# Performance work log

Measured on AMD Instinct MI355X. Metric: run time of the kernel, lower is better.

The kernel has to match this reference:

```python
import jax, jax.numpy as jnp
from jax import lax
import numpy as np

B, T, F, H, L = 256, 512, 16, 256, 2


def _lstm_layer(x, w_ih, w_hh, b_ih, b_hh):
    # x: [B, T, in]; w_ih: [4H, in]; w_hh: [4H, H]; biases: [4H]
    # PyTorch gate order: i, f, g, o
    x_proj = jnp.einsum('bti,gi->btg', x, w_ih) + b_ih + b_hh  # [B, T, 4H]
    h0 = jnp.zeros((x.shape[0], w_hh.shape[1]), x.dtype)
    c0 = h0

    def step(carry, xp):
        h, c = carry
        gates = xp + h @ w_hh.T  # [B, 4H]
        i, f, g, o = jnp.split(gates, 4, axis=-1)
        c = jax.nn.sigmoid(f) * c + jax.nn.sigmoid(i) * jnp.tanh(g)
        h = jax.nn.sigmoid(o) * jnp.tanh(c)
        return (h, c), h

    _, hs = lax.scan(step, (h0, c0), jnp.swapaxes(x_proj, 0, 1))  # [T, B, H]
    return jnp.swapaxes(hs, 0, 1)  # [B, T, H]


def setup_inputs() -> dict:
    key = jax.random.key(0)
    ks = jax.random.split(key, 16)
    x = jax.random.normal(ks[0], (B, T, F), dtype=jnp.float32)
    lengths = jax.random.randint(ks[1], (B,), 1, T + 1)  # in [1, T]
    s = 1.0 / np.sqrt(H)
    u = lambda k, shape: jax.random.uniform(k, shape, jnp.float32, -s, s)
    inp = {'x': x, 'lengths': lengths}
    in_dims = [F, H]
    for l in range(L):
        inp[f'w_ih{l}'] = u(ks[2 + 4 * l], (4 * H, in_dims[l]))
        inp[f'w_hh{l}'] = u(ks[3 + 4 * l], (4 * H, H))
        inp[f'b_ih{l}'] = u(ks[4 + 4 * l], (4 * H,))
        inp[f'b_hh{l}'] = u(ks[5 + 4 * l], (4 * H,))
    inp['fc_w'] = u(ks[10], (1, H))
    inp['fc_b'] = u(ks[11], (1,))
    return inp


def reference(x, lengths, w_ih0, w_hh0, b_ih0, b_hh0,
              w_ih1, w_hh1, b_ih1, b_hh1, fc_w, fc_b):
    # Packed LSTM: outputs at t >= length never influence last_outputs
    # (recurrence only flows forward in time), so running the dense
    # full-length LSTM and gathering at lengths-1 is mathematically identical.
    h = _lstm_layer(x, w_ih0, w_hh0, b_ih0, b_hh0)
    h = _lstm_layer(h, w_ih1, w_hh1, b_ih1, b_hh1)
    last = h[jnp.arange(h.shape[0]), lengths - 1]  # [B, H]
    return jax.nn.relu(last) @ fc_w.T + fc_b  # [B, 1]
```

## Files before the change

kernel.cpp:

```cpp
#include <hip/hip_runtime.h>
#include <hip/hip_fp16.h>


#define Tc 32
#define NCHUNK 16

#define OFF_IH0   0
#define OFF_B0    16384
#define OFF_B1    17408
#define OFF_C0S   18432
#define OFF_C1S   84480
#define OFF_H1S   150528
#define OFF_HLAST 216576
#define FP_END    282624
#define H_HH0  0
#define H_HH1  262144
#define H_IH1  524288
#define H_H0C  786432
#define H0SLOT 2113536
#define H_XP1  5013504
#define XPSLOT 8454144

#define SMEM_BYTES 66560

typedef _Float16 v2h __attribute__((ext_vector_type(2)));

__device__ __forceinline__ unsigned packh2(float a, float b) {
  __half2 h = __floats2half2_rn(a, b);
  return *(unsigned*)&h;
}
__device__ __forceinline__ float4 dot4(const float4 w, const v2h h, float4 acc) {
  const v2h* wg = (const v2h*)&w;
  acc.x = __builtin_amdgcn_fdot2(wg[0], h, acc.x, false);
  acc.y = __builtin_amdgcn_fdot2(wg[1], h, acc.y, false);
  acc.z = __builtin_amdgcn_fdot2(wg[2], h, acc.z, false);
  acc.w = __builtin_amdgcn_fdot2(wg[3], h, acc.w, false);
  return acc;
}
__device__ __forceinline__ float sigf(float x) {
  return __fdividef(1.f, 1.f + __expf(-x));
}
__device__ __forceinline__ float tanhf_fast(float x) {
  float ax = fabsf(x);
  float e = __expf(-2.f * ax);
  float t = __fdividef(1.f - e, 1.f + e);
  return copysignf(t, x);
}
__device__ __forceinline__ float4 f4fma(float4 a, float4 w, float s) {
  a.x = fmaf(w.x, s, a.x);
  a.y = fmaf(w.y, s, a.y);
  a.z = fmaf(w.z, s, a.z);
  a.w = fmaf(w.w, s, a.w);
  return a;
}
__device__ __forceinline__ float h2f(unsigned short s) {
  __half h = __builtin_bit_cast(__half, s);
  return __half2float(h);
}
__device__ __forceinline__ float4 cvt4(ushort4 v) {
  float4 r;
  r.x = h2f(v.x); r.y = h2f(v.y); r.z = h2f(v.z); r.w = h2f(v.w);
  return r;
}

__global__ __launch_bounds__(256) void prep_kernel(
    const float* __restrict__ w_ih0, const float* __restrict__ w_hh0,
    const float* __restrict__ b_ih0, const float* __restrict__ b_hh0,
    const float* __restrict__ w_ih1, const float* __restrict__ w_hh1,
    const float* __restrict__ b_ih1, const float* __restrict__ b_hh1,
    float* __restrict__ ws) {
  const int idx = blockIdx.x * blockDim.x + threadIdx.x;
  const int g = idx & 3, u = (idx >> 2) & 255, p = idx >> 10;
  const int j = g * 256 + u;
  unsigned* h16u = (unsigned*)(ws + FP_END);
  h16u[H_HH0 / 2 + idx] = packh2(w_hh0[j * 256 + 2 * p], w_hh0[j * 256 + 2 * p + 1]);
  h16u[H_HH1 / 2 + idx] = packh2(w_hh1[j * 256 + 2 * p], w_hh1[j * 256 + 2 * p + 1]);
  h16u[H_IH1 / 2 + idx] = packh2(w_ih1[j * 256 + 2 * p], w_ih1[j * 256 + 2 * p + 1]);
  if (idx < 16384) ws[OFF_IH0 + idx] = w_ih0[j * 16 + (idx >> 10)];
  if (idx < 1024) {
    ws[OFF_B0 + idx] = b_ih0[j] + b_hh0[j];
    ws[OFF_B1 + idx] = b_ih1[j] + b_hh1[j];
  }
}

__global__ __launch_bounds__(512) void fused_kernel(
    float* __restrict__ ws, const float* __restrict__ x,
    const int* __restrict__ lengths, int step) {
  extern __shared__ __align__(16) char smem_raw[];
  const int bid = blockIdx.x;
  const int tid = threadIdx.x;
  __half* h16 = (__half*)(ws + FP_END);
  unsigned short* h0cS = (unsigned short*)(h16 + H_H0C);
  unsigned short* xpS = (unsigned short*)(h16 + H_XP1);

  if (bid < 86) {
    if (step >= NCHUNK) return;
    const int kc = step;
    const int kh = tid >> 8, u = tid & 255;
    const int bg = bid * 3;
    unsigned short* hb = (unsigned short*)smem_raw;
    float* xsp = (float*)(smem_raw + 4096);
    float* scratch = (float*)(smem_raw + 4608);

    int len[3];
    #pragma unroll
    for (int b = 0; b < 3; ++b) len[b] = (bg + b < 256) ? lengths[bg + b] : 1;
    const int tmaxb = max(len[0], max(len[1], len[2]));
    if (kc * Tc >= tmaxb) return;
    const int tend = min(Tc, tmaxb - kc * Tc);
    const int slot = kc & 1, slotP = slot ^ 1;

    const float4* wq = (const float4*)(h16 + H_HH0) + (size_t)kh * 64 * 256 + u;
    const float4* wih = (const float4*)(ws + OFF_IH0) + kh * 8 * 256 + u;
    const float4 bias = ((const float4*)(ws + OFF_B0))[u];

    float c[3] = {0.f, 0.f, 0.f};
    if (kh == 0) {
      #pragma unroll
      for (int b = 0; b < 3; ++b) {
        unsigned short hv = 0;
        if (kc > 0) {
          hv = h0cS[(size_t)slotP * H0SLOT + ((size_t)(bg + b) * 32 + 31) * 256 + u];
          c[b] = ws[OFF_C0S + (bg + b) * 256 + u];
        }
        hb[0 * 768 + b * 256 + u] = hv;
      }
    }
    if (tid < 48) {
      int b = tid >> 4, i = tid & 15;
      int bb = min(bg + b, 255);
      xsp[0 * 48 + b * 16 + i] = x[(size_t)bb * 8192 + (kc * Tc) * 16 + i];
    }
    __syncthreads();

    for (int tc = 0; tc < tend; ++tc) {
      const int cur = tc & 1, nxt = cur ^ 1;
      float4 A0, A1, A2;
      if (kh == 0) { A0 = bias; A1 = bias; A2 = bias; }
      else { A0 = make_float4(0, 0, 0, 0); A1 = A0; A2 = A0; }

      #pragma unroll
      for (int ii = 0; ii < 8; ++ii) {
        float4 w = wih[ii * 256];
        A0 = f4fma(A0, w, xsp[cur * 48 + 0 * 16 + kh * 8 + ii]);
        A1 = f4fma(A1, w, xsp[cur * 48 + 1 * 16 + kh * 8 + ii]);
        A2 = f4fma(A2, w, xsp[cur * 48 + 2 * 16 + kh * 8 + ii]);
      }
      {
        const float4* h0r0 = (const float4*)(hb + cur * 768 + 0 * 256 + kh * 128);
        const float4* h0r1 = (const float4*)(hb + cur * 768 + 1 * 256 + kh * 128);
        const float4* h0r2 = (const float4*)(hb + cur * 768 + 2 * 256 + kh * 128);
        float4 wb[4], wn[4];
        #pragma unroll
        for (int p = 0; p < 4; ++p) wb[p] = wq[p * 256];
        for (int grp = 0; grp < 16; ++grp) {
          if (grp < 15) {
            #pragma unroll
            for (int p = 0; p < 4; ++p) wn[p] = wq[((grp + 1) * 4 + p) * 256];
          }
          float4 h40 = h0r0[grp], h41 = h0r1[grp], h42 = h0r2[grp];
          const v2h* hp0 = (const v2h*)&h40;
          const v2h* hp1 = (const v2h*)&h41;
          const v2h* hp2 = (const v2h*)&h42;
          #pragma unroll
          for (int p = 0; p < 4; ++p) {
            A0 = dot4(wb[p], hp0[p], A0);
            A1 = dot4(wb[p], hp1[p], A1);
            A2 = dot4(wb[p], hp2[p], A2);
          }
          #pragma unroll
          for (int p = 0; p < 4; ++p) wb[p] = wn[p];
        }
      }
      if (kh == 1) {
        #pragma unroll
        for (int g = 0; g < 4; ++g) {
          scratch[u * 13 + g] = ((const float*)&A0)[g];
          scratch[u * 13 + 4 + g] = ((const float*)&A1)[g];
          scratch[u * 13 + 8 + g] = ((const float*)&A2)[g];
        }
        if (tid < 256 + 48) {
          int bi = tid - 256, b = bi >> 4, i = bi & 15;
          int bb = min(bg + b, 255);
          int tn = min(kc * Tc + tc + 1, 511);
          xsp[nxt * 48 + b * 16 + i] = x[(size_t)bb * 8192 + tn * 16 + i];
        }
      }
      __syncthreads();
      if (kh == 0) {
        float4 B0, B1, B2;
        #pragma unroll
        for (int g = 0; g < 4; ++g) {
          ((float*)&B0)[g] = scratch[u * 13 + g];
          ((float*)&B1)[g] = scratch[u * 13 + 4 + g];
          ((float*)&B2)[g] = scratch[u * 13 + 8 + g];
        }
        A0 = f4fma(A0, B0, 1.f);
        A1 = f4fma(A1, B1, 1.f);
        A2 = f4fma(A2, B2, 1.f);
        float4 A[3] = {A0, A1, A2};
        #pragma unroll
        for (int b = 0; b < 3; ++b) {
          float ig = sigf(A[b].x), fg = sigf(A[b].y);
          float gg = tanhf_fast(A[b].z), og = sigf(A[b].w);
          c[b] = fg * c[b] + ig * gg;
          float h = og * tanhf_fast(c[b]);
          unsigned short hu = __half_as_ushort(__float2half(h));
          hb[nxt * 768 + b * 256 + u] = hu;
          h0cS[(size_t)slot * H0SLOT + ((size_t)(bg + b) * 32 + tc) * 256 + u] = hu;
        }
      }
      __syncthreads();
    }
    if (kh == 0) {
      #pragma unroll
      for (int b = 0; b < 3; ++b) ws[OFF_C0S + (bg + b) * 256 + u] = c[b];
    }

  } else if (bid < 172) {
    if (step < 2 || step >= NCHUNK + 2) return;
    const int kc = step - 2;
    const int kh = tid >> 8, u = tid & 255;
    const int bg = (bid - 86) * 3;
    unsigned short* h1b = (unsigned short*)smem_raw;
    float* scratch = (float*)(smem_raw + 4096);

    int len[3];
    #pragma unroll
    for (int b = 0; b < 3; ++b) len[b] = (bg + b < 256) ? lengths[bg + b] : 1;
    const int tmaxb = max(len[0], max(len[1], len[2]));
    if (kc * Tc >= tmaxb) return;
    const int tend = min(Tc, tmaxb - kc * Tc);
    const int slot = kc & 1;

    const float4* whP = (const float4*)(h16 + H_HH1) + (size_t)kh * 64 * 256 + u;

    float c[3] = {0.f, 0.f, 0.f}, hout[3] = {0.f, 0.f, 0.f};
    if (kh == 0) {
      #pragma unroll
      for (int b = 0; b < 3; ++b) {
        float hv = 0.f;
        if (kc > 0) {
          hv = ws[OFF_H1S + (bg + b) * 256 + u];
          c[b] = ws[OFF_C1S + (bg + b) * 256 + u];
        }
        h1b[0 * 768 + b * 256 + u] = __half_as_ushort(__float2half(hv));
      }
    }
    const unsigned short* xb =
        xpS + (size_t)slot * XPSLOT + (size_t)bg * 32768 + u * 4;
    ushort4 xc0, xc1, xc2;
    if (kh == 0) {
      xc0 = *(const ushort4*)(xb);
      xc1 = *(const ushort4*)(xb + 32768);
      xc2 = *(const ushort4*)(xb + 65536);
    }
    __syncthreads();

    for (int tc = 0; tc < tend; ++tc) {
      const int cur = tc & 1, nxt = cur ^ 1;
      float4 A0, A1, A2;
      ushort4 xn0, xn1, xn2;
      if (kh == 0) {
        A0 = cvt4(xc0); A1 = cvt4(xc1); A2 = cvt4(xc2);
        if (tc + 1 < tend) {
          xn0 = *(const ushort4*)(xb + (tc + 1) * 1024);
          xn1 = *(const ushort4*)(xb + 32768 + (tc + 1) * 1024);
          xn2 = *(const ushort4*)(xb + 65536 + (tc + 1) * 1024);
        }
      } else { A0 = make_float4(0, 0, 0, 0); A1 = A0; A2 = A0; }

      {
        const float4* r0 = (const float4*)(h1b + cur * 768 + 0 * 256 + kh * 128);
        const float4* r1 = (const float4*)(h1b + cur * 768 + 1 * 256 + kh * 128);
        const float4* r2 = (const float4*)(h1b + cur * 768 + 2 * 256 + kh * 128);
        float4 wb[4], wn[4];
        #pragma unroll
        for (int p = 0; p < 4; ++p) wb[p] = whP[p * 256];
        for (int grp = 0; grp < 16; ++grp) {
          if (grp < 15) {
            #pragma unroll
            for (int p = 0; p < 4; ++p) wn[p] = whP[((grp + 1) * 4 + p) * 256];
          }
          float4 v0 = r0[grp], v1 = r1[grp], v2 = r2[grp];
          const v2h* q0 = (const v2h*)&v0;
          const v2h* q1 = (const v2h*)&v1;
          const v2h* q2 = (const v2h*)&v2;
          #pragma unroll
          for (int p = 0; p < 4; ++p) {
            A0 = dot4(wb[p], q0[p], A0);
            A1 = dot4(wb[p], q1[p], A1);
            A2 = dot4(wb[p], q2[p], A2);
          }
          #pragma unroll
          for (int p = 0; p < 4; ++p) wb[p] = wn[p];
        }
      }
      if (kh == 1) {
        #pragma unroll
        for (int g = 0; g < 4; ++g) {
          scratch[u * 13 + g] = ((const float*)&A0)[g];
          scratch[u * 13 + 4 + g] = ((const float*)&A1)[g];
          scratch[u * 13 + 8 + g] = ((const float*)&A2)[g];
        }
      }
      __syncthreads();
      if (kh == 0) {
        float4 B0, B1, B2;
        #pragma unroll
        for (int g = 0; g < 4; ++g) {
          ((float*)&B0)[g] = scratch[u * 13 + g];
          ((float*)&B1)[g] = scratch[u * 13 + 4 + g];
          ((float*)&B2)[g] = scratch[u * 13 + 8 + g];
        }
        A0 = f4fma(A0, B0, 1.f);
        A1 = f4fma(A1, B1, 1.f);
        A2 = f4fma(A2, B2, 1.f);
        float4 A[3] = {A0, A1, A2};
        const int t = kc * Tc + tc;
        #pragma unroll
        for (int b = 0; b < 3; ++b) {
          float ig = sigf(A[b].x), fg = sigf(A[b].y);
          float gg = tanhf_fast(A[b].z), og = sigf(A[b].w);
          c[b] = fg * c[b] + ig * gg;
          float h = og * tanhf_fast(c[b]);
          hout[b] = h;
          h1b[nxt * 768 + b * 256 + u] = __half_as_ushort(__float2half(h));
          if (t == len[b] - 1) ws[OFF_HLAST + (bg + b) * 256 + u] = h;
        }
        xc0 = xn0; xc1 = xn1; xc2 = xn2;
      }
      __syncthreads();
    }
    if (kh == 0) {
      #pragma unroll
      for (int b = 0; b < 3; ++b) {
        ws[OFF_C1S + (bg + b) * 256 + u] = c[b];
        ws[OFF_H1S + (bg + b) * 256 + u] = hout[b];
      }
    }

  } else {
    if (step < 1 || step >= NCHUNK + 1) return;
    if (bid >= 236) return;
    const int kc = step - 1;
    const int gid = bid - 172;
    const int b0g = gid * 4;
    const int rt = tid & 63, wv = tid >> 6;
    __half2* hc2 = (__half2*)smem_raw;

    int lmax = 0;
    #pragma unroll
    for (int i = 0; i < 4; ++i) lmax = max(lmax, lengths[b0g + i]);
    if (kc * Tc >= lmax) return;
    const int slot = kc & 1;

    {
      const unsigned short* src =
          h0cS + (size_t)slot * H0SLOT + (size_t)b0g * 8192;
      const int cl = tid & 127, pg = tid >> 7;
      #pragma unroll
      for (int pp = 0; pp < 32; pp += 4) {
        const int p0 = pg * 32 + pp;
        uint4 v = *(const uint4*)(src + (size_t)cl * 256 + p0 * 2);
        unsigned* d = (unsigned*)hc2;
        d[(p0 + 0) * 128 + cl] = v.x;
        d[(p0 + 1) * 128 + cl] = v.y;
        d[(p0 + 2) * 128 + cl] = v.z;
        d[(p0 + 3) * 128 + cl] = v.w;
      }
    }
    __syncthreads();

    const __half* Wb = h16 + H_IH1;
    unsigned short* xdst = xpS + (size_t)slot * XPSLOT;
    #pragma unroll 1
    for (int rp = 0; rp < 2; ++rp) {
      #pragma unroll 1
      for (int cp = 0; cp < 2; ++cp) {
        const int uA = rp * 128 + rt, uB = uA + 64;
        const int c0 = cp * 64 + wv * 8;
        const float4 bA = ((const float4*)(ws + OFF_B1))[uA];
        const float4 bB = ((const float4*)(ws + OFF_B1))[uB];
        float accA[4][8], accB[4][8];
        #pragma unroll
        for (int g = 0; g < 4; ++g)
          #pragma unroll
          for (int cc = 0; cc < 8; ++cc) {
            accA[g][cc] = ((const float*)&bA)[g];
            accB[g][cc] = ((const float*)&bB)[g];
          }
        #pragma unroll 2
        for (int p = 0; p < 128; ++p) {
          float4 wA = *(const float4*)(Wb + (size_t)p * 2048 + uA * 8);
          float4 wB = *(const float4*)(Wb + (size_t)p * 2048 + uB * 8);
          float4 h0v = *(const float4*)(hc2 + p * 128 + c0);
          float4 h1v = *(const float4*)(hc2 + p * 128 + c0 + 4);
          const v2h* ga = (const v2h*)&wA;
          const v2h* gb = (const v2h*)&wB;
          const v2h* hv = (const v2h*)&h0v;
          const v2h* hw = (const v2h*)&h1v;
          #pragma unroll
          for (int g = 0; g < 4; ++g) {
            #pragma unroll
            for (int cc = 0; cc < 4; ++cc) {
              accA[g][cc] = __builtin_amdgcn_fdot2(ga[g], hv[cc], accA[g][cc], false);
              accA[g][cc + 4] = __builtin_amdgcn_fdot2(ga[g], hw[cc], accA[g][cc + 4], false);
              accB[g][cc] = __builtin_amdgcn_fdot2(gb[g], hv[cc], accB[g][cc], false);
              accB[g][cc + 4] = __builtin_amdgcn_fdot2(gb[g], hw[cc], accB[g][cc + 4], false);
            }
          }
        }
        #pragma unroll
        for (int cc = 0; cc < 8; ++cc) {
          const int col = c0 + cc;
          const size_t cb = ((size_t)(b0g + (col >> 5)) * 32 + (col & 31)) * 1024;
          ushort4 oA, oB;
          oA.x = __half_as_ushort(__float2half(accA[0][cc]));
          oA.y = __half_as_ushort(__float2half(accA[1][cc]));
          oA.z = __half_as_ushort(__float2half(accA[2][cc]));
          oA.w = __half_as_ushort(__float2half(accA[3][cc]));
          oB.x = __half_as_ushort(__float2half(accB[0][cc]));
          oB.y = __half_as_ushort(__float2half(accB[1][cc]));
          oB.z = __half_as_ushort(__float2half(accB[2][cc]));
          oB.w = __half_as_ushort(__float2half(accB[3][cc]));
          *(ushort4*)(xdst + cb + uA * 4) = oA;
          *(ushort4*)(xdst + cb + uB * 4) = oB;
        }
      }
    }
  }
}

__global__ __launch_bounds__(256) void fc_kernel(
    const float* __restrict__ ws, const float* __restrict__ fc_w,
    const float* __restrict__ fc_b, float* __restrict__ out) {
  __shared__ float red[256];
  const int tid = threadIdx.x;
  const int b = blockIdx.x;
  red[tid] = fmaxf(ws[OFF_HLAST + b * 256 + tid], 0.f) * fc_w[tid];
  __syncthreads();
  #pragma unroll
  for (int s = 128; s > 0; s >>= 1) {
    if (tid < s) red[tid] += red[tid + s];
    __syncthreads();
  }
  if (tid == 0) out[b] = red[0] + fc_b[0];
}

extern "C" void kernel_launch(void* const* d_in, const int* in_sizes, int n_in,
                              void* d_out, int out_size, void* d_ws, size_t ws_size,
                              hipStream_t stream) {
  const float* x     = (const float*)d_in[0];
  const int*   lens  = (const int*)d_in[1];
  const float* w_ih0 = (const float*)d_in[2];
  const float* w_hh0 = (const float*)d_in[3];
  const float* b_ih0 = (const float*)d_in[4];
  const float* b_hh0 = (const float*)d_in[5];
  const float* w_ih1 = (const float*)d_in[6];
  const float* w_hh1 = (const float*)d_in[7];
  const float* b_ih1 = (const float*)d_in[8];
  const float* b_hh1 = (const float*)d_in[9];
  const float* fc_w  = (const float*)d_in[10];
  const float* fc_b  = (const float*)d_in[11];
  float* out = (float*)d_out;
  float* ws  = (float*)d_ws;

  hipLaunchKernelGGL(prep_kernel, dim3(512), dim3(256), 0, stream,
                     w_ih0, w_hh0, b_ih0, b_hh0, w_ih1, w_hh1, b_ih1, b_hh1, ws);
  hipFuncSetAttribute(reinterpret_cast<const void*>(fused_kernel),
                      hipFuncAttributeMaxDynamicSharedMemorySize, SMEM_BYTES);
  for (int k = 0; k < NCHUNK + 2; ++k) {
    hipLaunchKernelGGL(fused_kernel, dim3(236), dim3(512), SMEM_BYTES, stream,
                       ws, x, lens, k);
  }
  hipLaunchKernelGGL(fc_kernel, dim3(256), dim3(256), 0, stream,
                     ws, fc_w, fc_b, out);
}
```

Baseline: 3.135 ms.

## Keep half of recurrent weights resident in registers, stage fp16 input weights in LDS

Each thread now loads half of its slice of the recurrent weight matrix (32 float4 of packed fp16) into registers once per chunk. The other half is streamed from global memory with a triple-buffered prefetch, which cuts per-timestep global weight traffic in both layer kernels. The layer-0 input projection weights and x are converted to fp16 and applied with fdot2, and those weights are staged in LDS. This adds register pressure under launch_bounds(512,2) and could cause spills, and fp16 x adds rounding error.

```diff
diff --git a/kernel.cpp b/kernel.cpp
--- a/kernel.cpp
+++ b/kernel.cpp
@@ -46,13 +46,6 @@
   float t = __fdividef(1.f - e, 1.f + e);
   return copysignf(t, x);
 }
-__device__ __forceinline__ float4 f4fma(float4 a, float4 w, float s) {
-  a.x = fmaf(w.x, s, a.x);
-  a.y = fmaf(w.y, s, a.y);
-  a.z = fmaf(w.z, s, a.z);
-  a.w = fmaf(w.w, s, a.w);
-  return a;
-}
 __device__ __forceinline__ float h2f(unsigned short s) {
   __half h = __builtin_bit_cast(__half, s);
   return __half2float(h);
@@ -61,6 +54,9 @@
   float4 r;
   r.x = h2f(v.x); r.y = h2f(v.y); r.z = h2f(v.z); r.w = h2f(v.w);
   return r;
+}
+__device__ __forceinline__ v2h u2h(unsigned v) {
+  return __builtin_bit_cast(v2h, v);
 }
 
 __global__ __launch_bounds__(256) void prep_kernel(
@@ -76,14 +72,17 @@
   h16u[H_HH0 / 2 + idx] = packh2(w_hh0[j * 256 + 2 * p], w_hh0[j * 256 + 2 * p + 1]);
   h16u[H_HH1 / 2 + idx] = packh2(w_hh1[j * 256 + 2 * p], w_hh1[j * 256 + 2 * p + 1]);
   h16u[H_IH1 / 2 + idx] = packh2(w_ih1[j * 256 + 2 * p], w_ih1[j * 256 + 2 * p + 1]);
-  if (idx < 16384) ws[OFF_IH0 + idx] = w_ih0[j * 16 + (idx >> 10)];
+  if (idx < 8192) {
+    ((unsigned*)(ws + OFF_IH0))[idx] =
+        packh2(w_ih0[j * 16 + 2 * p], w_ih0[j * 16 + 2 * p + 1]);
+  }
   if (idx < 1024) {
     ws[OFF_B0 + idx] = b_ih0[j] + b_hh0[j];
     ws[OFF_B1 + idx] = b_ih1[j] + b_hh1[j];
   }
 }
 
-__global__ __launch_bounds__(512) void fused_kernel(
+__global__ __launch_bounds__(512, 2) void fused_kernel(
     float* __restrict__ ws, const float* __restrict__ x,
     const int* __restrict__ lengths, int step) {
   extern __shared__ __align__(16) char smem_raw[];
@@ -99,8 +98,9 @@
     const int kh = tid >> 8, u = tid & 255;
     const int bg = bid * 3;
     unsigned short* hb = (unsigned short*)smem_raw;
-    float* xsp = (float*)(smem_raw + 4096);
-    float* scratch = (float*)(smem_raw + 4608);
+    unsigned* xsp = (unsigned*)(smem_raw + 4096);
+    float* scratch = (float*)(smem_raw + 4352);
+    float4* wxl = (float4*)(smem_raw + 18048);
 
     int len[3];
     #pragma unroll
@@ -110,8 +110,17 @@
     const int tend = min(Tc, tmaxb - kc * Tc);
     const int slot = kc & 1, slotP = slot ^ 1;
 
-    const float4* wq = (const float4*)(h16 + H_HH0) + (size_t)kh * 64 * 256 + u;
-    const float4* wih = (const float4*)(ws + OFF_IH0) + kh * 8 * 256 + u;
+    {
+      const float4* gwx = (const float4*)(ws + OFF_IH0);
+      #pragma unroll
+      for (int e = 0; e < 4; ++e) wxl[tid + e * 512] = gwx[tid + e * 512];
+    }
+
+    const float4* wqR = (const float4*)(h16 + H_HH0) + (size_t)(kh * 64) * 256 + u;
+    float4 wreg[32];
+    #pragma unroll
+    for (int p = 0; p < 32; ++p) wreg[p] = wqR[p * 256];
+    const float4* wqS = wqR + 32 * 256;
     const float4 bias = ((const float4*)(ws + OFF_B0))[u];
 
     float c[3] = {0.f, 0.f, 0.f};
@@ -126,10 +135,11 @@
         hb[0 * 768 + b * 256 + u] = hv;
       }
     }
-    if (tid < 48) {
-      int b = tid >> 4, i = tid & 15;
+    if (tid < 24) {
+      int b = tid >> 3, i = tid & 7;
       int bb = min(bg + b, 255);
-      xsp[0 * 48 + b * 16 + i] = x[(size_t)bb * 8192 + (kc * Tc) * 16 + i];
+      const float* xp = x + (size_t)bb * 8192 + (kc * Tc) * 16;
+      xsp[0 * 24 + b * 8 + i] = packh2(xp[2 * i], xp[2 * i + 1]);
     }
     __syncthreads();
 
@@ -140,38 +150,61 @@
       else { A0 = make_float4(0, 0, 0, 0); A1 = A0; A2 = A0; }
 
       #pragma unroll
-      for (int ii = 0; ii < 8; ++ii) {
-        float4 w = wih[ii * 256];
-        A0 = f4fma(A0, w, xsp[cur * 48 + 0 * 16 + kh * 8 + ii]);
-        A1 = f4fma(A1, w, xsp[cur * 48 + 1 * 16 + kh * 8 + ii]);
-        A2 = f4fma(A2, w, xsp[cur * 48 + 2 * 16 + kh * 8 + ii]);
+      for (int p = 0; p < 4; ++p) {
+        float4 w = wxl[(kh * 4 + p) * 256 + u];
+        v2h x0 = u2h(xsp[cur * 24 + 0 * 8 + kh * 4 + p]);
+        v2h x1 = u2h(xsp[cur * 24 + 1 * 8 + kh * 4 + p]);
+        v2h x2 = u2h(xsp[cur * 24 + 2 * 8 + kh * 4 + p]);
+        A0 = dot4(w, x0, A0);
+        A1 = dot4(w, x1, A1);
+        A2 = dot4(w, x2, A2);
+      }
+
+      const float4* h0r0 = (const float4*)(hb + cur * 768 + 0 * 256 + kh * 128);
+      const float4* h0r1 = (const float4*)(hb + cur * 768 + 1 * 256 + kh * 128);
+      const float4* h0r2 = (const float4*)(hb + cur * 768 + 2 * 256 + kh * 128);
+
+      #pragma unroll
+      for (int grp = 0; grp < 8; ++grp) {
+        float4 h40 = h0r0[grp], h41 = h0r1[grp], h42 = h0r2[grp];
+        const v2h* hp0 = (const v2h*)&h40;
+        const v2h* hp1 = (const v2h*)&h41;
+        const v2h* hp2 = (const v2h*)&h42;
+        #pragma unroll
+        for (int q = 0; q < 4; ++q) {
+          A0 = dot4(wreg[grp * 4 + q], hp0[q], A0);
+          A1 = dot4(wreg[grp * 4 + q], hp1[q], A1);
+          A2 = dot4(wreg[grp * 4 + q], hp2[q], A2);
+        }
       }
       {
-        const float4* h0r0 = (const float4*)(hb + cur * 768 + 0 * 256 + kh * 128);
-        const float4* h0r1 = (const float4*)(hb + cur * 768 + 1 * 256 + kh * 128);
-        const float4* h0r2 = (const float4*)(hb + cur * 768 + 2 * 256 + kh * 128);
-        float4 wb[4], wn[4];
-        #pragma unroll
-        for (int p = 0; p < 4; ++p) wb[p] = wq[p * 256];
-        for (int grp = 0; grp < 16; ++grp) {
-          if (grp < 15) {
+        float4 B[3][4];
+        #pragma unroll
+        for (int p = 0; p < 4; ++p) {
+          B[0][p] = wqS[p * 256];
+          B[1][p] = wqS[(4 + p) * 256];
+        }
+        #pragma unroll
+        for (int g = 0; g < 8; ++g) {
+          if (g + 2 < 8) {
             #pragma unroll
-            for (int p = 0; p < 4; ++p) wn[p] = wq[((grp + 1) * 4 + p) * 256];
+            for (int p = 0; p < 4; ++p)
+              B[(g + 2) % 3][p] = wqS[((g + 2) * 4 + p) * 256];
           }
-          float4 h40 = h0r0[grp], h41 = h0r1[grp], h42 = h0r2[grp];
+          const float4* wbuf = B[g % 3];
+          float4 h40 = h0r0[8 + g], h41 = h0r1[8 + g], h42 = h0r2[8 + g];
           const v2h* hp0 = (const v2h*)&h40;
           const v2h* hp1 = (const v2h*)&h41;
           const v2h* hp2 = (const v2h*)&h42;
           #pragma unroll
-          for (int p = 0; p < 4; ++p) {
-            A0 = dot4(wb[p], hp0[p], A0);
-            A1 = dot4(wb[p], hp1[p], A1);
-            A2 = dot4(wb[p], hp2[p], A2);
+          for (int q = 0; q < 4; ++q) {
+            A0 = dot4(wbuf[q], hp0[q], A0);
+            A1 = dot4(wbuf[q], hp1[q], A1);
+            A2 = dot4(wbuf[q], hp2[q], A2);
           }
-          #pragma unroll
-          for (int p = 0; p < 4; ++p) wb[p] = wn[p];
-        }
-      }
+        }
+      }
+
       if (kh == 1) {
         #pragma unroll
         for (int g = 0; g < 4; ++g) {
@@ -179,11 +212,12 @@
           scratch[u * 13 + 4 + g] = ((const float*)&A1)[g];
           scratch[u * 13 + 8 + g] = ((const float*)&A2)[g];
         }
-        if (tid < 256 + 48) {
-          int bi = tid - 256, b = bi >> 4, i = bi & 15;
+        if (tid < 256 + 24) {
+          int bi = tid - 256, b = bi >> 3, i = bi & 7;
           int bb = min(bg + b, 255);
           int tn = min(kc * Tc + tc + 1, 511);
-          xsp[nxt * 48 + b * 16 + i] = x[(size_t)bb * 8192 + tn * 16 + i];
+          const float* xp = x + (size_t)bb * 8192 + tn * 16;
+          xsp[nxt * 24 + b * 8 + i] = packh2(xp[2 * i], xp[2 * i + 1]);
         }
       }
       __syncthreads();
@@ -195,9 +229,9 @@
           ((float*)&B1)[g] = scratch[u * 13 + 4 + g];
           ((float*)&B2)[g] = scratch[u * 13 + 8 + g];
         }
-        A0 = f4fma(A0, B0, 1.f);
-        A1 = f4fma(A1, B1, 1.f);
-        A2 = f4fma(A2, B2, 1.f);
+        A0.x += B0.x; A0.y += B0.y; A0.z += B0.z; A0.w += B0.w;
+        A1.x += B1.x; A1.y += B1.y; A1.z += B1.z; A1.w += B1.w;
+        A2.x += B2.x; A2.y += B2.y; A2.z += B2.z; A2.w += B2.w;
         float4 A[3] = {A0, A1, A2};
         #pragma unroll
         for (int b = 0; b < 3; ++b) {
@@ -233,7 +267,11 @@
     const int tend = min(Tc, tmaxb - kc * Tc);
     const int slot = kc & 1;
 
-    const float4* whP = (const float4*)(h16 + H_HH1) + (size_t)kh * 64 * 256 + u;
+    const float4* wqR = (const float4*)(h16 + H_HH1) + (size_t)(kh * 64) * 256 + u;
+    float4 wreg[32];
+    #pragma unroll
+    for (int p = 0; p < 32; ++p) wreg[p] = wqR[p * 256];
+    const float4* wqS = wqR + 32 * 256;
 
     float c[3] = {0.f, 0.f, 0.f}, hout[3] = {0.f, 0.f, 0.f};
     if (kh == 0) {
@@ -270,32 +308,51 @@
         }
       } else { A0 = make_float4(0, 0, 0, 0); A1 = A0; A2 = A0; }
 
+      const float4* r0 = (const float4*)(h1b + cur * 768 + 0 * 256 + kh * 128);
+      const float4* r1 = (const float4*)(h1b + cur * 768 + 1 * 256 + kh * 128);
+      const float4* r2 = (const float4*)(h1b + cur * 768 + 2 * 256 + kh * 128);
+
+      #pragma unroll
+      for (int grp = 0; grp < 8; ++grp) {
+        float4 h40 = r0[grp], h41 = r1[grp], h42 = r2[grp];
+        const v2h* hp0 = (const v2h*)&h40;
+        const v2h* hp1 = (const v2h*)&h41;
+        const v2h* hp2 = (const v2h*)&h42;
+        #pragma unroll
+        for (int q = 0; q < 4; ++q) {
+          A0 = dot4(wreg[grp * 4 + q], hp0[q], A0);
+          A1 = dot4(wreg[grp * 4 + q], hp1[q], A1);
+          A2 = dot4(wreg[grp * 4 + q], hp2[q], A2);
+        }
+      }
       {
-        const float4* r0 = (const float4*)(h1b + cur * 768 + 0 * 256 + kh * 128);
-        const float4* r1 = (const float4*)(h1b + cur * 768 + 1 * 256 + kh * 128);
-        const float4* r2 = (const float4*)(h1b + cur * 768 + 2 * 256 + kh * 128);
-        float4 wb[4], wn[4];
-        #pragma unroll
-        for (int p = 0; p < 4; ++p) wb[p] = whP[p * 256];
-        for (int grp = 0; grp < 16; ++grp) {
-          if (grp < 15) {
+        float4 B[3][4];
+        #pragma unroll
+        for (int p = 0; p < 4; ++p) {
+          B[0][p] = wqS[p * 256];
+          B[1][p] = wqS[(4 + p) * 256];
+        }
+        #pragma unroll
+        for (int g = 0; g < 8; ++g) {
+          if (g + 2 < 8) {
             #pragma unroll
-            for (int p = 0; p < 4; ++p) wn[p] = whP[((grp + 1) * 4 + p) * 256];
+            for (int p = 0; p < 4; ++p)
+              B[(g + 2) % 3][p] = wqS[((g + 2) * 4 + p) * 256];
           }
-          float4 v0 = r0[grp], v1 = r1[grp], v2 = r2[grp];
-          const v2h* q0 = (const v2h*)&v0;
-          const v2h* q1 = (const v2h*)&v1;
-          const v2h* q2 = (const v2h*)&v2;
+          const float4* wbuf = B[g % 3];
+          float4 h40 = r0[8 + g], h41 = r1[8 + g], h42 = r2[8 + g];
+          const v2h* hp0 = (const v2h*)&h40;
+          const v2h* hp1 = (const v2h*)&h41;
+          const v2h* hp2 = (const v2h*)&h42;
           #pragma unroll
-          for (int p = 0; p < 4; ++p) {
-            A0 = dot4(wb[p], q0[p], A0);
-            A1 = dot4(wb[p], q1[p], A1);
-            A2 = dot4(wb[p], q2[p], A2);
+          for (int q = 0; q < 4; ++q) {
+            A0 = dot4(wbuf[q], hp0[q], A0);
+            A1 = dot4(wbuf[q], hp1[q], A1);
+            A2 = dot4(wbuf[q], hp2[q], A2);
           }
-          #pragma unroll
-          for (int p = 0; p < 4; ++p) wb[p] = wn[p];
-        }
-      }
+        }
+      }
+
       if (kh == 1) {
         #pragma unroll
         for (int g = 0; g < 4; ++g) {
@@ -313,9 +370,9 @@
           ((float*)&B1)[g] = scratch[u * 13 + 4 + g];
           ((float*)&B2)[g] = scratch[u * 13 + 8 + g];
         }
-        A0 = f4fma(A0, B0, 1.f);
-        A1 = f4fma(A1, B1, 1.f);
-        A2 = f4fma(A2, B2, 1.f);
+        A0.x += B0.x; A0.y += B0.y; A0.z += B0.z; A0.w += B0.w;
+        A1.x += B1.x; A1.y += B1.y; A1.z += B1.z; A1.w += B1.w;
+        A2.x += B2.x; A2.y += B2.y; A2.z += B2.z; A2.w += B2.w;
         float4 A[3] = {A0, A1, A2};
         const int t = kc * Tc + tc;
         #pragma unroll
```

Result: no change. 3.145 ms (+0.3%).
